# Kernel optimization log

Hardware: AMD Instinct MI355X
Metric: run time of the kernel (lower is better)

Reference implementation:

```python
import jax, jax.numpy as jnp
import numpy as np

N_ACTIVE = 200000
N_IN = 64
N_OUT = 64
K = 27          # filter volume (3^3)
R = 100000      # rulebook pairs per filter offset


def setup_inputs() -> dict:
    key = jax.random.key(0)
    k1, k2, k3, k4 = jax.random.split(key, 4)
    std = (2.0 / (N_IN * K)) ** 0.5
    features = jax.random.normal(k1, (N_ACTIVE, N_IN), dtype=jnp.float32)
    weight = jax.random.normal(k2, (N_IN * K, N_OUT), dtype=jnp.float32) * std
    bias = jnp.zeros((N_OUT,), dtype=jnp.float32)
    in_idx = jax.random.randint(k3, (K, R), 0, N_ACTIVE, dtype=jnp.int64 if jax.config.jax_enable_x64 else jnp.int32)
    out_idx = jax.random.randint(k4, (K, R), 0, N_ACTIVE, dtype=jnp.int64 if jax.config.jax_enable_x64 else jnp.int32)
    return {"features": features, "weight": weight, "bias": bias,
            "in_idx": in_idx, "out_idx": out_idx}


def reference(features, weight, bias, in_idx, out_idx):
    # Rulebook-based submanifold sparse convolution:
    # for each filter offset k: gather inputs, matmul with weight slice,
    # scatter-accumulate into output sites. Bias added once per active site.
    n_active, n_in = features.shape
    k = in_idx.shape[0]
    W = weight.reshape(k, n_in, -1)            # [K, nIn, nOut]
    gathered = features[in_idx]                # [K, R, nIn]  (irregular gather)
    contrib = jnp.einsum('kri,kio->kro', gathered, W)  # grouped matmul
    out = jnp.zeros((n_active, W.shape[2]), dtype=features.dtype)
    out = out.at[out_idx.reshape(-1)].add(contrib.reshape(-1, W.shape[2]))
    return out + bias
```

## Files before the change

kernel.cpp:

```cpp
#include <hip/hip_runtime.h>
#include <stdint.h>

#define N_ACTIVE 200000
#define N_IN 64
#define N_OUT 64
#define K_FILT 27
#define R_PAIRS 100000
#define TOTP (K_FILT * R_PAIRS)
#define NSLOT (N_ACTIVE * K_FILT)

#define CF_BLOCKS (N_ACTIVE * N_IN / 8 / 256)
#define CW_BLOCKS K_FILT

typedef __bf16 bf16x8 __attribute__((ext_vector_type(8)));
typedef float f32x4 __attribute__((ext_vector_type(4)));

__global__ __launch_bounds__(256) void prep_convert(
    const float* __restrict__ feat, __bf16* __restrict__ featb,
    const float* __restrict__ wsrc, __bf16* __restrict__ wt)
{
    int bb = blockIdx.x, t = threadIdx.x;
    if (bb < CF_BLOCKS) {
        int i = bb * 256 + t;
        const f32x4* src = reinterpret_cast<const f32x4*>(feat) + 2 * (size_t)i;
        f32x4 v0 = __builtin_nontemporal_load(src);
        f32x4 v1 = __builtin_nontemporal_load(src + 1);
        bf16x8 o;
        o[0] = (__bf16)v0[0]; o[1] = (__bf16)v0[1]; o[2] = (__bf16)v0[2]; o[3] = (__bf16)v0[3];
        o[4] = (__bf16)v1[0]; o[5] = (__bf16)v1[1]; o[6] = (__bf16)v1[2]; o[7] = (__bf16)v1[3];
        reinterpret_cast<bf16x8*>(featb)[i] = o;
    } else {
        int kf = bb - CF_BLOCKS;
        const float* wk = wsrc + kf * 4096;
        __bf16* wo = wt + kf * 4096;
        int o = t >> 2, i0 = (t & 3) * 16;
        bf16x8 a, b;
        #pragma unroll
        for (int j = 0; j < 8; ++j) a[j] = (__bf16)wk[(i0 + j) * 64 + o];
        #pragma unroll
        for (int j = 0; j < 8; ++j) b[j] = (__bf16)wk[(i0 + 8 + j) * 64 + o];
        *reinterpret_cast<bf16x8*>(wo + o * 64 + i0) = a;
        *reinterpret_cast<bf16x8*>(wo + o * 64 + i0 + 8) = b;
    }
}

__global__ __launch_bounds__(256) void claim_pairs(
    const int* __restrict__ in_idx, const int* __restrict__ out_idx,
    int* __restrict__ slotCnt,
    int* __restrict__ slot1, int* __restrict__ slot2, int* __restrict__ slot3,
    int2* __restrict__ ovf, int* __restrict__ ovfCur)
{
    int p = blockIdx.x * 256 + threadIdx.x;
    if (p >= TOTP) return;
    unsigned k = (unsigned)p / (unsigned)R_PAIRS;
    int row = out_idx[p];
    int iv  = in_idx[p];
    int slot = row * K_FILT + (int)k;
    int c = atomicAdd(&slotCnt[slot], 1);
    if (c == 0)      slot1[slot] = iv;
    else if (c == 1) slot2[slot] = iv;
    else if (c == 2) slot3[slot] = iv;
    else {
        int q = atomicAdd(ovfCur, 1);
        ovf[q] = make_int2(slot, iv);
    }
}

__global__ __launch_bounds__(256) void conv_slots(
    const __bf16* __restrict__ featb,
    const __bf16* __restrict__ wtb,
    const float* __restrict__ bias,
    const int* __restrict__ slotCnt,
    const int* __restrict__ slot1, const int* __restrict__ slot2,
    const int* __restrict__ slot3,
    float* __restrict__ out)
{
    const int t = threadIdx.x;
    const int w = t >> 6;
    const int lane = t & 63;
    const int lrow = lane & 15;
    const int kg   = lane >> 4;
    const int rowBase = blockIdx.x * 64 + w * 16;
    const int slotBase = (rowBase + lrow) * K_FILT;

    f32x4 acc0 = {0.f,0.f,0.f,0.f}, acc1 = acc0, acc2 = acc0, acc3 = acc0;

    const float b0 = bias[lrow], b1 = bias[16 + lrow],
                b2 = bias[32 + lrow], b3 = bias[48 + lrow];

    for (int kf = 0; kf < K_FILT; ++kf) {
        const __bf16* wk = wtb + kf * 4096;
        bf16x8 bf00 = *reinterpret_cast<const bf16x8*>(wk + (lrow)      * 64 + kg * 8);
        bf16x8 bf01 = *reinterpret_cast<const bf16x8*>(wk + (lrow)      * 64 + 32 + kg * 8);
        bf16x8 bf10 = *reinterpret_cast<const bf16x8*>(wk + (16 + lrow) * 64 + kg * 8);
        bf16x8 bf11 = *reinterpret_cast<const bf16x8*>(wk + (16 + lrow) * 64 + 32 + kg * 8);
        bf16x8 bf20 = *reinterpret_cast<const bf16x8*>(wk + (32 + lrow) * 64 + kg * 8);
        bf16x8 bf21 = *reinterpret_cast<const bf16x8*>(wk + (32 + lrow) * 64 + 32 + kg * 8);
        bf16x8 bf30 = *reinterpret_cast<const bf16x8*>(wk + (48 + lrow) * 64 + kg * 8);
        bf16x8 bf31 = *reinterpret_cast<const bf16x8*>(wk + (48 + lrow) * 64 + 32 + kg * 8);

        int slot = slotBase + kf;
        int c  = slotCnt[slot];
        int i1 = slot1[slot];
        int addr = (c > 0) ? i1 : 0;
        const __bf16* ap = featb + (size_t)addr * 64 + kg * 8;
        bf16x8 x0 = *reinterpret_cast<const bf16x8*>(ap);
        bf16x8 x1 = *reinterpret_cast<const bf16x8*>(ap + 32);

        if (__any(c > 1)) {
            if (c > 1) {
                int i2 = slot2[slot];
                const __bf16* bp = featb + (size_t)i2 * 64 + kg * 8;
                bf16x8 y0 = *reinterpret_cast<const bf16x8*>(bp);
                bf16x8 y1 = *reinterpret_cast<const bf16x8*>(bp + 32);
                float f0[8], f1[8];
                #pragma unroll
                for (int j = 0; j < 8; ++j) {
                    f0[j] = (float)x0[j] + (float)y0[j];
                    f1[j] = (float)x1[j] + (float)y1[j];
                }
                if (c > 2) {
                    int i3 = slot3[slot];
                    const __bf16* cp = featb + (size_t)i3 * 64 + kg * 8;
                    bf16x8 z0 = *reinterpret_cast<const bf16x8*>(cp);
                    bf16x8 z1 = *reinterpret_cast<const bf16x8*>(cp + 32);
                    #pragma unroll
                    for (int j = 0; j < 8; ++j) {
                        f0[j] += (float)z0[j];
                        f1[j] += (float)z1[j];
                    }
                }
                #pragma unroll
                for (int j = 0; j < 8; ++j) {
                    x0[j] = (__bf16)f0[j];
                    x1[j] = (__bf16)f1[j];
                }
            }
        }
        if (c <= 0) {
            #pragma unroll
            for (int j = 0; j < 8; ++j) { x0[j] = (__bf16)0.f; x1[j] = (__bf16)0.f; }
        }

        acc0 = __builtin_amdgcn_mfma_f32_16x16x32_bf16(x0, bf00, acc0, 0, 0, 0);
        acc0 = __builtin_amdgcn_mfma_f32_16x16x32_bf16(x1, bf01, acc0, 0, 0, 0);
        acc1 = __builtin_amdgcn_mfma_f32_16x16x32_bf16(x0, bf10, acc1, 0, 0, 0);
        acc1 = __builtin_amdgcn_mfma_f32_16x16x32_bf16(x1, bf11, acc1, 0, 0, 0);
        acc2 = __builtin_amdgcn_mfma_f32_16x16x32_bf16(x0, bf20, acc2, 0, 0, 0);
        acc2 = __builtin_amdgcn_mfma_f32_16x16x32_bf16(x1, bf21, acc2, 0, 0, 0);
        acc3 = __builtin_amdgcn_mfma_f32_16x16x32_bf16(x0, bf30, acc3, 0, 0, 0);
        acc3 = __builtin_amdgcn_mfma_f32_16x16x32_bf16(x1, bf31, acc3, 0, 0, 0);
    }

    #pragma unroll
    for (int r = 0; r < 4; ++r) {
        int gr = rowBase + kg * 4 + r;
        float* orow = out + (size_t)gr * 64;
        orow[lrow]      = acc0[r] + b0;
        orow[16 + lrow] = acc1[r] + b1;
        orow[32 + lrow] = acc2[r] + b2;
        orow[48 + lrow] = acc3[r] + b3;
    }
}

__global__ __launch_bounds__(64) void ovf_cleanup(
    const __bf16* __restrict__ featb, const __bf16* __restrict__ wtb,
    const int2* __restrict__ ovf, const int* __restrict__ ovfCur,
    float* __restrict__ out)
{
    const int n = *ovfCur;
    const int lane = threadIdx.x;
    for (int e = blockIdx.x; e < n; e += gridDim.x) {
        int2 v = ovf[e];
        int slot = v.x, in = v.y;
        int row = slot / K_FILT;
        int kf  = slot - row * K_FILT;
        const __bf16* fp = featb + (size_t)in * 64;
        const __bf16* wp = wtb + kf * 4096 + lane * 64;
        float s = 0.f;
        #pragma unroll
        for (int j = 0; j < 8; ++j) {
            bf16x8 fv = *reinterpret_cast<const bf16x8*>(fp + j * 8);
            bf16x8 wv = *reinterpret_cast<const bf16x8*>(wp + j * 8);
            #pragma unroll
            for (int q = 0; q < 8; ++q) s += (float)fv[q] * (float)wv[q];
        }
        atomicAdd(&out[(size_t)row * 64 + lane], s);
    }
}

extern "C" void kernel_launch(void* const* d_in, const int* in_sizes, int n_in,
                              void* d_out, int out_size, void* d_ws, size_t ws_size,
                              hipStream_t stream) {
    const float* feat    = (const float*)d_in[0];
    const float* weight  = (const float*)d_in[1];
    const float* bias    = (const float*)d_in[2];
    const int*   in_idx  = (const int*)d_in[3];
    const int*   out_idx = (const int*)d_in[4];
    float* out = (float*)d_out;

    char* wsb = (char*)d_ws;
    __bf16* featb  = (__bf16*)wsb;
    __bf16* wtb    = (__bf16*)(wsb + 25600000);
    int*  slotCnt  = (int*) (wsb + 25600000 + 221184);
    int*  slot1    = slotCnt + NSLOT;
    int*  slot2    = slot1 + NSLOT;
    int*  slot3    = slot2 + NSLOT;
    int*  ovfCur   = slot3 + NSLOT;
    int2* ovf      = (int2*)(ovfCur + 4);

    hipMemsetAsync(slotCnt, 0, (size_t)NSLOT * 4, stream);
    hipMemsetAsync(ovfCur, 0, 16, stream);

    prep_convert<<<dim3(CF_BLOCKS + CW_BLOCKS), dim3(256), 0, stream>>>(
        feat, featb, weight, wtb);
    claim_pairs<<<dim3((TOTP + 255) / 256), dim3(256), 0, stream>>>(
        in_idx, out_idx, slotCnt, slot1, slot2, slot3, ovf, ovfCur);
    conv_slots<<<dim3(N_ACTIVE / 64), dim3(256), 0, stream>>>(
        featb, wtb, bias, slotCnt, slot1, slot2, slot3, out);
    ovf_cleanup<<<dim3(2048), dim3(64), 0, stream>>>(featb, wtb, ovf, ovfCur, out);
}
```

Baseline: 665.7 us.

## Fuse prep and claim kernels, make slot gather branchless with nontemporal hints

Merges the bf16 conversion and rulebook-claim kernels into one launch so their work can overlap and one launch boundary disappears. The conv kernel now issues all three slot gathers unconditionally (masked to row 0 / zero) and sums them branch-free, adds an occupancy hint and partial unroll, and uses nontemporal loads/stores for streaming index and output traffic. The branchless gather adds extra loads on mostly empty slots and may raise register pressure.

```diff
diff --git a/kernel.cpp b/kernel.cpp
--- a/kernel.cpp
+++ b/kernel.cpp
@@ -11,13 +11,18 @@
 
 #define CF_BLOCKS (N_ACTIVE * N_IN / 8 / 256)
 #define CW_BLOCKS K_FILT
+#define CL_BLOCKS ((TOTP + 255) / 256)
 
 typedef __bf16 bf16x8 __attribute__((ext_vector_type(8)));
 typedef float f32x4 __attribute__((ext_vector_type(4)));
 
-__global__ __launch_bounds__(256) void prep_convert(
+__global__ __launch_bounds__(256) void prep_fused(
     const float* __restrict__ feat, __bf16* __restrict__ featb,
-    const float* __restrict__ wsrc, __bf16* __restrict__ wt)
+    const float* __restrict__ wsrc, __bf16* __restrict__ wt,
+    const int* __restrict__ in_idx, const int* __restrict__ out_idx,
+    int* __restrict__ slotCnt,
+    int* __restrict__ slot1, int* __restrict__ slot2, int* __restrict__ slot3,
+    int2* __restrict__ ovf, int* __restrict__ ovfCur)
 {
     int bb = blockIdx.x, t = threadIdx.x;
     if (bb < CF_BLOCKS) {
@@ -29,7 +34,7 @@
         o[0] = (__bf16)v0[0]; o[1] = (__bf16)v0[1]; o[2] = (__bf16)v0[2]; o[3] = (__bf16)v0[3];
         o[4] = (__bf16)v1[0]; o[5] = (__bf16)v1[1]; o[6] = (__bf16)v1[2]; o[7] = (__bf16)v1[3];
         reinterpret_cast<bf16x8*>(featb)[i] = o;
-    } else {
+    } else if (bb < CF_BLOCKS + CW_BLOCKS) {
         int kf = bb - CF_BLOCKS;
         const float* wk = wsrc + kf * 4096;
         __bf16* wo = wt + kf * 4096;
@@ -41,32 +46,26 @@
         for (int j = 0; j < 8; ++j) b[j] = (__bf16)wk[(i0 + 8 + j) * 64 + o];
         *reinterpret_cast<bf16x8*>(wo + o * 64 + i0) = a;
         *reinterpret_cast<bf16x8*>(wo + o * 64 + i0 + 8) = b;
-    }
-}
-
-__global__ __launch_bounds__(256) void claim_pairs(
-    const int* __restrict__ in_idx, const int* __restrict__ out_idx,
-    int* __restrict__ slotCnt,
-    int* __restrict__ slot1, int* __restrict__ slot2, int* __restrict__ slot3,
-    int2* __restrict__ ovf, int* __restrict__ ovfCur)
-{
-    int p = blockIdx.x * 256 + threadIdx.x;
-    if (p >= TOTP) return;
-    unsigned k = (unsigned)p / (unsigned)R_PAIRS;
-    int row = out_idx[p];
-    int iv  = in_idx[p];
-    int slot = row * K_FILT + (int)k;
-    int c = atomicAdd(&slotCnt[slot], 1);
-    if (c == 0)      slot1[slot] = iv;
-    else if (c == 1) slot2[slot] = iv;
-    else if (c == 2) slot3[slot] = iv;
-    else {
-        int q = atomicAdd(ovfCur, 1);
-        ovf[q] = make_int2(slot, iv);
-    }
-}
-
-__global__ __launch_bounds__(256) void conv_slots(
+    } else {
+        int p = (bb - CF_BLOCKS - CW_BLOCKS) * 256 + t;
+        if (p < TOTP) {
+            unsigned k = (unsigned)p / (unsigned)R_PAIRS;
+            int row = __builtin_nontemporal_load(&out_idx[p]);
+            int iv  = __builtin_nontemporal_load(&in_idx[p]);
+            int slot = row * K_FILT + (int)k;
+            int c = atomicAdd(&slotCnt[slot], 1);
+            if (c == 0)      slot1[slot] = iv;
+            else if (c == 1) slot2[slot] = iv;
+            else if (c == 2) slot3[slot] = iv;
+            else {
+                int q = atomicAdd(ovfCur, 1);
+                ovf[q] = make_int2(slot, iv);
+            }
+        }
+    }
+}
+
+__global__ __launch_bounds__(256, 3) void conv_slots(
     const __bf16* __restrict__ featb,
     const __bf16* __restrict__ wtb,
     const float* __restrict__ bias,
@@ -80,86 +79,76 @@
     const int lane = t & 63;
     const int lrow = lane & 15;
     const int kg   = lane >> 4;
+    const int kgo  = kg * 8;
     const int rowBase = blockIdx.x * 64 + w * 16;
     const int slotBase = (rowBase + lrow) * K_FILT;
 
     f32x4 acc0 = {0.f,0.f,0.f,0.f}, acc1 = acc0, acc2 = acc0, acc3 = acc0;
-
     const float b0 = bias[lrow], b1 = bias[16 + lrow],
                 b2 = bias[32 + lrow], b3 = bias[48 + lrow];
-
+    const bf16x8 zero8 = {};
+
+    #pragma unroll 3
     for (int kf = 0; kf < K_FILT; ++kf) {
+        const int slot = slotBase + kf;
+        int c  = __builtin_nontemporal_load(&slotCnt[slot]);
+        int s1 = __builtin_nontemporal_load(&slot1[slot]);
+        int s2 = __builtin_nontemporal_load(&slot2[slot]);
+        int s3 = __builtin_nontemporal_load(&slot3[slot]);
+        int a1 = (c > 0) ? s1 : 0;
+        int a2 = (c > 1) ? s2 : 0;
+        int a3 = (c > 2) ? s3 : 0;
+
+        const __bf16* p1 = featb + (size_t)a1 * 64 + kgo;
+        const __bf16* p2 = featb + (size_t)a2 * 64 + kgo;
+        const __bf16* p3 = featb + (size_t)a3 * 64 + kgo;
+        bf16x8 x0 = *reinterpret_cast<const bf16x8*>(p1);
+        bf16x8 x1 = *reinterpret_cast<const bf16x8*>(p1 + 32);
+        bf16x8 y0 = *reinterpret_cast<const bf16x8*>(p2);
+        bf16x8 y1 = *reinterpret_cast<const bf16x8*>(p2 + 32);
+        bf16x8 z0 = *reinterpret_cast<const bf16x8*>(p3);
+        bf16x8 z1 = *reinterpret_cast<const bf16x8*>(p3 + 32);
+
         const __bf16* wk = wtb + kf * 4096;
-        bf16x8 bf00 = *reinterpret_cast<const bf16x8*>(wk + (lrow)      * 64 + kg * 8);
-        bf16x8 bf01 = *reinterpret_cast<const bf16x8*>(wk + (lrow)      * 64 + 32 + kg * 8);
-        bf16x8 bf10 = *reinterpret_cast<const bf16x8*>(wk + (16 + lrow) * 64 + kg * 8);
-        bf16x8 bf11 = *reinterpret_cast<const bf16x8*>(wk + (16 + lrow) * 64 + 32 + kg * 8);
-        bf16x8 bf20 = *reinterpret_cast<const bf16x8*>(wk + (32 + lrow) * 64 + kg * 8);
-        bf16x8 bf21 = *reinterpret_cast<const bf16x8*>(wk + (32 + lrow) * 64 + 32 + kg * 8);
-        bf16x8 bf30 = *reinterpret_cast<const bf16x8*>(wk + (48 + lrow) * 64 + kg * 8);
-        bf16x8 bf31 = *reinterpret_cast<const bf16x8*>(wk + (48 + lrow) * 64 + 32 + kg * 8);
-
-        int slot = slotBase + kf;
-        int c  = slotCnt[slot];
-        int i1 = slot1[slot];
-        int addr = (c > 0) ? i1 : 0;
-        const __bf16* ap = featb + (size_t)addr * 64 + kg * 8;
-        bf16x8 x0 = *reinterpret_cast<const bf16x8*>(ap);
-        bf16x8 x1 = *reinterpret_cast<const bf16x8*>(ap + 32);
-
-        if (__any(c > 1)) {
-            if (c > 1) {
-                int i2 = slot2[slot];
-                const __bf16* bp = featb + (size_t)i2 * 64 + kg * 8;
-                bf16x8 y0 = *reinterpret_cast<const bf16x8*>(bp);
-                bf16x8 y1 = *reinterpret_cast<const bf16x8*>(bp + 32);
-                float f0[8], f1[8];
-                #pragma unroll
-                for (int j = 0; j < 8; ++j) {
-                    f0[j] = (float)x0[j] + (float)y0[j];
-                    f1[j] = (float)x1[j] + (float)y1[j];
-                }
-                if (c > 2) {
-                    int i3 = slot3[slot];
-                    const __bf16* cp = featb + (size_t)i3 * 64 + kg * 8;
-                    bf16x8 z0 = *reinterpret_cast<const bf16x8*>(cp);
-                    bf16x8 z1 = *reinterpret_cast<const bf16x8*>(cp + 32);
-                    #pragma unroll
-                    for (int j = 0; j < 8; ++j) {
-                        f0[j] += (float)z0[j];
-                        f1[j] += (float)z1[j];
-                    }
-                }
-                #pragma unroll
-                for (int j = 0; j < 8; ++j) {
-                    x0[j] = (__bf16)f0[j];
-                    x1[j] = (__bf16)f1[j];
-                }
-            }
+        bf16x8 bf00 = *reinterpret_cast<const bf16x8*>(wk + (lrow)      * 64 + kgo);
+        bf16x8 bf01 = *reinterpret_cast<const bf16x8*>(wk + (lrow)      * 64 + 32 + kgo);
+        bf16x8 bf10 = *reinterpret_cast<const bf16x8*>(wk + (16 + lrow) * 64 + kgo);
+        bf16x8 bf11 = *reinterpret_cast<const bf16x8*>(wk + (16 + lrow) * 64 + 32 + kgo);
+        bf16x8 bf20 = *reinterpret_cast<const bf16x8*>(wk + (32 + lrow) * 64 + kgo);
+        bf16x8 bf21 = *reinterpret_cast<const bf16x8*>(wk + (32 + lrow) * 64 + 32 + kgo);
+        bf16x8 bf30 = *reinterpret_cast<const bf16x8*>(wk + (48 + lrow) * 64 + kgo);
+        bf16x8 bf31 = *reinterpret_cast<const bf16x8*>(wk + (48 + lrow) * 64 + 32 + kgo);
+
+        x0 = (c > 0) ? x0 : zero8;  x1 = (c > 0) ? x1 : zero8;
+        y0 = (c > 1) ? y0 : zero8;  y1 = (c > 1) ? y1 : zero8;
+        z0 = (c > 2) ? z0 : zero8;  z1 = (c > 2) ? z1 : zero8;
+        bf16x8 A0, A1;
+        #pragma unroll
+        for (int j = 0; j < 8; ++j) {
+            float f0 = (float)x0[j] + (float)y0[j] + (float)z0[j];
+            float f1 = (float)x1[j] + (float)y1[j] + (float)z1[j];
+            A0[j] = (__bf16)f0;
+            A1[j] = (__bf16)f1;
         }
-        if (c <= 0) {
-            #pragma unroll
-            for (int j = 0; j < 8; ++j) { x0[j] = (__bf16)0.f; x1[j] = (__bf16)0.f; }
-        }
-
-        acc0 = __builtin_amdgcn_mfma_f32_16x16x32_bf16(x0, bf00, acc0, 0, 0, 0);
-        acc0 = __builtin_amdgcn_mfma_f32_16x16x32_bf16(x1, bf01, acc0, 0, 0, 0);
-        acc1 = __builtin_amdgcn_mfma_f32_16x16x32_bf16(x0, bf10, acc1, 0, 0, 0);
-        acc1 = __builtin_amdgcn_mfma_f32_16x16x32_bf16(x1, bf11, acc1, 0, 0, 0);
-        acc2 = __builtin_amdgcn_mfma_f32_16x16x32_bf16(x0, bf20, acc2, 0, 0, 0);
-        acc2 = __builtin_amdgcn_mfma_f32_16x16x32_bf16(x1, bf21, acc2, 0, 0, 0);
-        acc3 = __builtin_amdgcn_mfma_f32_16x16x32_bf16(x0, bf30, acc3, 0, 0, 0);
-        acc3 = __builtin_amdgcn_mfma_f32_16x16x32_bf16(x1, bf31, acc3, 0, 0, 0);
+
+        acc0 = __builtin_amdgcn_mfma_f32_16x16x32_bf16(A0, bf00, acc0, 0, 0, 0);
+        acc0 = __builtin_amdgcn_mfma_f32_16x16x32_bf16(A1, bf01, acc0, 0, 0, 0);
+        acc1 = __builtin_amdgcn_mfma_f32_16x16x32_bf16(A0, bf10, acc1, 0, 0, 0);
+        acc1 = __builtin_amdgcn_mfma_f32_16x16x32_bf16(A1, bf11, acc1, 0, 0, 0);
+        acc2 = __builtin_amdgcn_mfma_f32_16x16x32_bf16(A0, bf20, acc2, 0, 0, 0);
+        acc2 = __builtin_amdgcn_mfma_f32_16x16x32_bf16(A1, bf21, acc2, 0, 0, 0);
+        acc3 = __builtin_amdgcn_mfma_f32_16x16x32_bf16(A0, bf30, acc3, 0, 0, 0);
+        acc3 = __builtin_amdgcn_mfma_f32_16x16x32_bf16(A1, bf31, acc3, 0, 0, 0);
     }
 
     #pragma unroll
     for (int r = 0; r < 4; ++r) {
         int gr = rowBase + kg * 4 + r;
         float* orow = out + (size_t)gr * 64;
-        orow[lrow]      = acc0[r] + b0;
-        orow[16 + lrow] = acc1[r] + b1;
-        orow[32 + lrow] = acc2[r] + b2;
-        orow[48 + lrow] = acc3[r] + b3;
+        __builtin_nontemporal_store(acc0[r] + b0, &orow[lrow]);
+        __builtin_nontemporal_store(acc1[r] + b1, &orow[16 + lrow]);
+        __builtin_nontemporal_store(acc2[r] + b2, &orow[32 + lrow]);
+        __builtin_nontemporal_store(acc3[r] + b3, &orow[48 + lrow]);
     }
 }
 
@@ -212,10 +201,9 @@
     hipMemsetAsync(slotCnt, 0, (size_t)NSLOT * 4, stream);
     hipMemsetAsync(ovfCur, 0, 16, stream);
 
-    prep_convert<<<dim3(CF_BLOCKS + CW_BLOCKS), dim3(256), 0, stream>>>(
-        feat, featb, weight, wtb);
-    claim_pairs<<<dim3((TOTP + 255) / 256), dim3(256), 0, stream>>>(
-        in_idx, out_idx, slotCnt, slot1, slot2, slot3, ovf, ovfCur);
+    prep_fused<<<dim3(CF_BLOCKS + CW_BLOCKS + CL_BLOCKS), dim3(256), 0, stream>>>(
+        feat, featb, weight, wtb, in_idx, out_idx,
+        slotCnt, slot1, slot2, slot3, ovf, ovfCur);
     conv_slots<<<dim3(N_ACTIVE / 64), dim3(256), 0, stream>>>(
         featb, wtb, bias, slotCnt, slot1, slot2, slot3, out);
     ovf_cleanup<<<dim3(2048), dim3(64), 0, stream>>>(featb, wtb, ovf, ovfCur, out);
```

Result: no change. 664.5 us (-0.2%).
